# Kernel tuning notes

Measured on AMD Instinct MI355X. Metric: run time of the kernel, lower is better.

Reference implementation:

```python
import jax, jax.numpy as jnp
import numpy as np


def _adaptive_pool_mat(n_in, n_out):
    # torch AdaptiveAvgPool2d bin edges: start=floor(i*n_in/n_out), end=ceil((i+1)*n_in/n_out)
    M = np.zeros((n_out, n_in), np.float32)
    for i in range(n_out):
        s = (i * n_in) // n_out
        e = -(-((i + 1) * n_in) // n_out)
        M[i, s:e] = 1.0 / (e - s)
    return jnp.asarray(M)


def _bilinear_mat(n_out, n_in):
    # torch F.interpolate bilinear, align_corners=False, as a (n_out, n_in) matrix
    M = np.zeros((n_out, n_in), np.float32)
    scale = n_in / n_out
    for i in range(n_out):
        src = max((i + 0.5) * scale - 0.5, 0.0)
        i0 = min(int(np.floor(src)), n_in - 1)
        w = src - i0
        i1 = min(i0 + 1, n_in - 1)
        M[i, i0] += 1.0 - w
        M[i, i1] += w
    return jnp.asarray(M)


def _bn(x, g, b, m, v):
    # inference-mode BatchNorm2d over channel axis 1 of (B,C,H,W)
    inv = g / jnp.sqrt(v + 1e-5)
    return x * inv[None, :, None, None] + (b - m * inv)[None, :, None, None]


def _selective_scan(u, delta, A, Bs, Cs, D):
    # u, delta: (B,K,Di,L); A: (K,Di,N); Bs, Cs: (B,K,N,L); D: (K,Di)
    def step(h, inp):
        u_l, d_l, B_l, C_l = inp  # (B,K,Di), (B,K,Di), (B,K,N), (B,K,N)
        h = h * jnp.exp(d_l[..., None] * A) + (d_l * u_l)[..., None] * B_l[:, :, None, :]
        return h, jnp.einsum('bkdn,bkn->bkd', h, C_l)

    h0 = jnp.zeros(u.shape[:3] + (A.shape[-1],), u.dtype)
    xs = (u.transpose(3, 0, 1, 2), delta.transpose(3, 0, 1, 2),
          Bs.transpose(3, 0, 1, 2), Cs.transpose(3, 0, 1, 2))
    _, ys = jax.lax.scan(step, h0, xs)  # ys: (L,B,K,Di)
    return ys.transpose(1, 2, 3, 0) + D[None, :, :, None] * u


def _ss2d(x, in_proj_w, conv_w, conv_b, x_proj_w, dt_w, dt_b, A_logs, Ds, ln_g, ln_b, out_proj_w):
    # x: (B,H,W,d_model); VMamba SS2D with K=4 scan directions
    B, H, W, _ = x.shape
    K, N = 4, 16
    R = dt_w.shape[-1]
    Di = in_proj_w.shape[0] // 2
    xz = jnp.einsum('bhwc,ec->bhwe', x, in_proj_w)
    xi, z = jnp.split(xz, 2, axis=-1)
    xc = xi.transpose(0, 3, 1, 2)  # (B,Di,H,W)
    xc = jax.lax.conv_general_dilated(xc, conv_w, (1, 1), [(1, 1), (1, 1)],
                                      dimension_numbers=('NCHW', 'OIHW', 'NCHW'),
                                      feature_group_count=Di)
    xc = jax.nn.silu(xc + conv_b[None, :, None, None])
    L = H * W
    x_hw = xc.reshape(B, Di, L)
    x_wh = xc.transpose(0, 1, 3, 2).reshape(B, Di, L)
    xs2 = jnp.stack([x_hw, x_wh], axis=1)
    xs4 = jnp.concatenate([xs2, jnp.flip(xs2, axis=-1)], axis=1)  # (B,4,Di,L)
    x_dbl = jnp.einsum('bkdl,kcd->bkcl', xs4, x_proj_w)
    dts, Bm, Cm = jnp.split(x_dbl, [R, R + N], axis=2)
    delta = jax.nn.softplus(jnp.einsum('bkrl,kdr->bkdl', dts, dt_w) + dt_b[None, :, :, None])
    A = -jnp.exp(A_logs).reshape(K, Di, N)
    out_y = _selective_scan(xs4, delta, A, Bm, Cm, Ds.reshape(K, Di))  # (B,4,Di,L)
    inv_y = jnp.flip(out_y[:, 2:4], axis=-1)
    wh_y = out_y[:, 1].reshape(B, Di, W, H).transpose(0, 1, 3, 2).reshape(B, Di, L)
    invwh_y = inv_y[:, 1].reshape(B, Di, W, H).transpose(0, 1, 3, 2).reshape(B, Di, L)
    y = out_y[:, 0] + inv_y[:, 0] + wh_y + invwh_y  # (B,Di,L)
    y = y.transpose(0, 2, 1).reshape(B, H, W, Di)
    mu = jnp.mean(y, -1, keepdims=True)
    var = jnp.var(y, -1, keepdims=True)
    y = (y - mu) / jnp.sqrt(var + 1e-5) * ln_g + ln_b  # out_norm (LayerNorm)
    y = y * jax.nn.silu(z)
    return jnp.einsum('bhwd,cd->bhwc', y, out_proj_w)


def _forward(x, pool_w, pool_b, bn_g, bn_b, bn_m, bn_v, in_proj_w, conv_w, conv_b,
             x_proj_w, dt_w, dt_b, A_logs, Ds, ln_g, ln_b, out_proj_w,
             cbr_w, cbr_b, cbr_g, cbr_beta, cbr_m, cbr_v):
    B, C, H, W = x.shape
    pool_scales = [1, 5, 9, 13]  # generate_arithmetic_sequence(1, 16, 4)
    outs = [x]
    # pool layer 0: conv1x1 -> BN -> ReLU -> global avg pool -> upsample (constant)
    y0 = jnp.einsum('bchw,dc->bdhw', x, pool_w[0]) + pool_b[0][None, :, None, None]
    y0 = jax.nn.relu(_bn(y0, bn_g[0], bn_b[0], bn_m[0], bn_v[0]))
    y0 = jnp.mean(y0, axis=(2, 3), keepdims=True)
    outs.append(jnp.broadcast_to(y0, (B, y0.shape[1], H, W)))
    # pool layers 1..3: adaptive avg pool -> conv1x1 -> BN -> ReLU -> bilinear upsample
    for i, s in enumerate(pool_scales[1:], start=1):
        Mh, Mw = _adaptive_pool_mat(H, s), _adaptive_pool_mat(W, s)
        p = jnp.einsum('bchw,ph,qw->bcpq', x, Mh, Mw)
        p = jnp.einsum('bcpq,dc->bdpq', p, pool_w[i]) + pool_b[i][None, :, None, None]
        p = jax.nn.relu(_bn(p, bn_g[i], bn_b[i], bn_m[i], bn_v[i]))
        Uh, Uw = _bilinear_mat(H, s), _bilinear_mat(W, s)
        outs.append(jnp.einsum('bcpq,hp,wq->bchw', p, Uh, Uw))
    feat = jnp.concatenate(outs, axis=1)  # (B, dim*4 + in_chs = 1024, H, W)
    y = _ss2d(feat.transpose(0, 2, 3, 1), in_proj_w, conv_w, conv_b, x_proj_w,
              dt_w, dt_b, A_logs, Ds, ln_g, ln_b, out_proj_w)
    y = y.transpose(0, 3, 1, 2)
    # cbr: conv1x1 -> BN -> GELU
    y = jnp.einsum('bchw,dc->bdhw', y, cbr_w) + cbr_b[None, :, None, None]
    y = _bn(y, cbr_g, cbr_beta, cbr_m, cbr_v)
    return jax.nn.gelu(y, approximate=False)


def setup_inputs():
    key = jax.random.key(0)
    ks = jax.random.split(key, 20)
    B, C, H, W = 4, 512, 16, 16
    dim, P = 128, 4
    dm = dim * P + C            # 1024
    Di, K, N, R = 2 * dm, 4, 16, dm // 16  # 2048, 4, 16, 64
    f = jax.random.normal
    return {
        'x': f(ks[0], (B, C, H, W), jnp.float32),
        'pool_w': f(ks[1], (P, dim, C), jnp.float32) * 0.05,
        'pool_b': f(ks[2], (P, dim), jnp.float32) * 0.05,
        'bn_g': jnp.ones((P, dim), jnp.float32),
        'bn_b': jnp.zeros((P, dim), jnp.float32),
        'bn_m': f(ks[3], (P, dim), jnp.float32) * 0.1,
        'bn_v': jax.random.uniform(ks[4], (P, dim), jnp.float32, 0.5, 1.5),
        'in_proj_w': f(ks[5], (2 * Di, dm), jnp.float32) * 0.02,
        'conv_w': f(ks[6], (Di, 1, 3, 3), jnp.float32) * 0.1,
        'conv_b': f(ks[7], (Di,), jnp.float32) * 0.05,
        'x_proj_w': f(ks[8], (K, R + 2 * N, Di), jnp.float32) * 0.02,
        'dt_w': f(ks[9], (K, Di, R), jnp.float32) * 0.05,
        'dt_b': f(ks[10], (K, Di), jnp.float32) * 0.1,
        'A_logs': jax.random.uniform(ks[11], (K * Di, N), jnp.float32),
        'Ds': f(ks[12], (K * Di,), jnp.float32) * 0.1,
        'ln_g': jnp.ones((Di,), jnp.float32),
        'ln_b': jnp.zeros((Di,), jnp.float32),
        'out_proj_w': f(ks[13], (dm, Di), jnp.float32) * 0.02,
        'cbr_w': f(ks[14], (dim, dm), jnp.float32) * 0.05,
        'cbr_b': f(ks[15], (dim,), jnp.float32) * 0.05,
        'cbr_g': jnp.ones((dim,), jnp.float32),
        'cbr_beta': jnp.zeros((dim,), jnp.float32),
        'cbr_m': f(ks[16], (dim,), jnp.float32) * 0.1,
        'cbr_v': jax.random.uniform(ks[17], (dim,), jnp.float32, 0.5, 1.5),
    }


def reference(x, pool_w, pool_b, bn_g, bn_b, bn_m, bn_v, in_proj_w, conv_w, conv_b,
              x_proj_w, dt_w, dt_b, A_logs, Ds, ln_g, ln_b, out_proj_w,
              cbr_w, cbr_b, cbr_g, cbr_beta, cbr_m, cbr_v):
    return _forward(x, pool_w, pool_b, bn_g, bn_b, bn_m, bn_v, in_proj_w, conv_w, conv_b,
                    x_proj_w, dt_w, dt_b, A_logs, Ds, ln_g, ln_b, out_proj_w,
                    cbr_w, cbr_b, cbr_g, cbr_beta, cbr_m, cbr_v)
```

## Files before the change

kernel.cpp:

```cpp
#include <hip/hip_runtime.h>
#include <hip/hip_bf16.h>
#include <math.h>

#define Bsz 4
#define Cin 512
#define Hh 16
#define Ww 16
#define Lsp 256
#define DIM 128
#define DM 1024
#define DI 2048
#define KK 4
#define NST 16
#define RR 64
#define PW 384
#define NCH 4
#define CHUNK 64

#define OFF_FEAT    0u
#define SZ_FEAT     (Bsz*Lsp*DM)
#define OFF_POOLED  (OFF_FEAT + SZ_FEAT)
#define SZ_POOLED   (Bsz*Cin*275)
#define OFF_PCONV   (OFF_POOLED + SZ_POOLED)
#define SZ_PCONV    (Bsz*275*DIM)
#define OFF_Y0M     (OFF_PCONV + SZ_PCONV)
#define SZ_Y0M      (Bsz*DIM)
#define OFF_XZ      (OFF_Y0M + SZ_Y0M)
#define SZ_XZ       (Bsz*Lsp*2*DI)
#define OFF_XCT     (OFF_XZ + SZ_XZ)
#define SZ_XCT      (Bsz*Lsp*DI)
#define OFF_XDBL    (OFF_XCT + SZ_XCT)
#define SZ_XDBL     (Bsz*Lsp*PW)
#define OFF_DELTA   (OFF_XDBL + SZ_XDBL)
#define SZ_DELTA    (Bsz*KK*Lsp*DI)
#define OFF_OUTY    (OFF_DELTA + SZ_DELTA)
#define SZ_OUTY     (Bsz*KK*Lsp*DI)
#define OFF_YG      (OFF_OUTY + SZ_OUTY)
#define SZ_YG       (Bsz*Lsp*DI)
#define OFF_O1      (OFF_YG + SZ_YG)
#define SZ_O1       (Bsz*Lsp*DM)
#define OFF_O2      (OFF_O1 + SZ_O1)
#define SZ_O2       (Bsz*Lsp*DIM)
#define WS_FLOATS   (OFF_O2 + SZ_O2)

typedef __attribute__((ext_vector_type(8))) short short8;
typedef __attribute__((ext_vector_type(4))) float f32x4;

__device__ __forceinline__ short f2bf(float x) {
  __hip_bfloat16 h = __float2bfloat16(x);
  short s;
  __builtin_memcpy(&s, &h, 2);
  return s;
}
__device__ __forceinline__ float bf2f(short s) {
  unsigned u = ((unsigned)(unsigned short)s) << 16;
  float f;
  __builtin_memcpy(&f, &u, 4);
  return f;
}
__device__ __forceinline__ float unpack_lo(unsigned v) {
  unsigned u = v << 16; float f; __builtin_memcpy(&f, &u, 4); return f;
}
__device__ __forceinline__ float unpack_hi(unsigned v) {
  unsigned u = v & 0xffff0000u; float f; __builtin_memcpy(&f, &u, 4); return f;
}

__global__ __launch_bounds__(256) void f2bf5_kernel(
    const float* __restrict__ s0, short* __restrict__ d0,
    const float* __restrict__ s1, short* __restrict__ d1,
    const float* __restrict__ s2, short* __restrict__ d2,
    const float* __restrict__ s3, short* __restrict__ d3,
    const float* __restrict__ s4, short* __restrict__ d4) {
  int blk = blockIdx.x;
  const float* src; short* dst; int base;
  if (blk < 2048)      { src = s0; dst = d0; base = blk; }
  else if (blk < 2432) { src = s1; dst = d1; base = blk - 2048; }
  else if (blk < 3456) { src = s2; dst = d2; base = blk - 2432; }
  else if (blk < 3520) { src = s3; dst = d3; base = blk - 3456; }
  else                 { src = s4; dst = d4; base = blk - 3520; }
  int i = (base*256 + threadIdx.x)*8;
  float4 a = *(const float4*)(src + i);
  float4 b = *(const float4*)(src + i + 4);
  short8 o;
  o[0]=f2bf(a.x); o[1]=f2bf(a.y); o[2]=f2bf(a.z); o[3]=f2bf(a.w);
  o[4]=f2bf(b.x); o[5]=f2bf(b.y); o[6]=f2bf(b.z); o[7]=f2bf(b.w);
  *(short8*)(dst + i) = o;
}

__global__ __launch_bounds__(256) void pool0_kernel(
    const float* __restrict__ x, const float* __restrict__ pw, const float* __restrict__ pb,
    const float* __restrict__ g, const float* __restrict__ bb,
    const float* __restrict__ m, const float* __restrict__ v, float* __restrict__ y0m) {
  int bd = blockIdx.x;
  int b = bd >> 7, d = bd & 127;
  int l = threadIdx.x;
  const float* xb = x + (b*Cin)*Lsp + l;
  const float* w = pw + d*Cin;
  float a0 = 0.f, a1 = 0.f, a2 = 0.f, a3 = 0.f;
  #pragma unroll 4
  for (int c = 0; c < Cin; c += 4) {
    float4 wv = *(const float4*)(w + c);
    a0 += xb[(c+0)*Lsp] * wv.x;
    a1 += xb[(c+1)*Lsp] * wv.y;
    a2 += xb[(c+2)*Lsp] * wv.z;
    a3 += xb[(c+3)*Lsp] * wv.w;
  }
  float s = (a0 + a1) + (a2 + a3) + pb[d];
  float inv = g[d] * rsqrtf(v[d] + 1e-5f);
  s = s*inv + (bb[d] - m[d]*inv);
  s = fmaxf(s, 0.f);
  __shared__ float red[256];
  red[l] = s; __syncthreads();
  for (int off = 128; off > 0; off >>= 1) {
    if (l < off) red[l] += red[l+off];
    __syncthreads();
  }
  if (l == 0) y0m[bd] = red[0] * (1.f/256.f);
}

__device__ __forceinline__ void decode_pos(int pos, int& s, int& pp, int& qq, int& layer) {
  if (pos < 25)       { s = 5;  layer = 1; int t = pos;       pp = t/5;  qq = t%5;  }
  else if (pos < 106) { s = 9;  layer = 2; int t = pos - 25;  pp = t/9;  qq = t%9;  }
  else                { s = 13; layer = 3; int t = pos - 106; pp = t/13; qq = t%13; }
}

__global__ void pool_avg_kernel(const float* __restrict__ x, float* __restrict__ pooled) {
  int bc = blockIdx.x;
  int pos = threadIdx.x;
  if (pos >= 275) return;
  int s, pp, qq, layer;
  decode_pos(pos, s, pp, qq, layer);
  int hs = (pp*Hh)/s, he = ((pp+1)*Hh + s-1)/s;
  int ws = (qq*Ww)/s, we = ((qq+1)*Ww + s-1)/s;
  const float* xb = x + (size_t)bc*Lsp;
  float acc = 0.f;
  for (int hh = hs; hh < he; ++hh)
    for (int ww2 = ws; ww2 < we; ++ww2)
      acc += xb[hh*Ww + ww2];
  pooled[(size_t)bc*275 + pos] = acc / (float)((he-hs)*(we-ws));
}

__global__ void pconv_kernel(const float* __restrict__ pooled, const float* __restrict__ pw,
    const float* __restrict__ pb, const float* __restrict__ g, const float* __restrict__ bb,
    const float* __restrict__ m, const float* __restrict__ v, float* __restrict__ pconv) {
  int bp = blockIdx.x;
  int b = bp / 275, pos = bp % 275;
  int d = threadIdx.x;
  int s, pp, qq, layer;
  decode_pos(pos, s, pp, qq, layer);
  const float* pc = pooled + b*Cin*275 + pos;
  const float* w = pw + (layer*DIM + d)*Cin;
  float a0 = 0.f, a1 = 0.f, a2 = 0.f, a3 = 0.f;
  #pragma unroll 4
  for (int c = 0; c < Cin; c += 4) {
    float4 wv = *(const float4*)(w + c);
    a0 += pc[(c+0)*275] * wv.x;
    a1 += pc[(c+1)*275] * wv.y;
    a2 += pc[(c+2)*275] * wv.z;
    a3 += pc[(c+3)*275] * wv.w;
  }
  float acc = (a0 + a1) + (a2 + a3) + pb[layer*DIM + d];
  int ld = layer*DIM + d;
  float inv = g[ld] * rsqrtf(v[ld] + 1e-5f);
  acc = acc*inv + (bb[ld] - m[ld]*inv);
  pconv[bp*DIM + d] = fmaxf(acc, 0.f);
}

__global__ __launch_bounds__(256) void xT_kernel(const float* __restrict__ x,
    short* __restrict__ featB) {
  int b = blockIdx.z;
  int c0 = blockIdx.x*32, l0 = blockIdx.y*32;
  __shared__ float t[32][33];
  int tx = threadIdx.x & 31, ty = threadIdx.x >> 5;
  #pragma unroll
  for (int i = 0; i < 4; ++i) {
    int c = c0 + ty + i*8;
    t[ty + i*8][tx] = x[((size_t)b*Cin + c)*Lsp + l0 + tx];
  }
  __syncthreads();
  #pragma unroll
  for (int i = 0; i < 4; ++i) {
    int l = l0 + ty + i*8;
    featB[(size_t)(b*Lsp + l)*DM + c0 + tx] = f2bf(t[tx][ty + i*8]);
  }
}

__global__ __launch_bounds__(256) void feat_fill(const float* __restrict__ y0m,
    const float* __restrict__ pconv, short* __restrict__ featB) {
  int bl = blockIdx.x;
  int b = bl >> 8, l = bl & 255;
  int h = l >> 4, w = l & 15;
  for (int cc = threadIdx.x; cc < 512; cc += 256) {
    float val;
    if (cc < 128) {
      val = y0m[b*DIM + cc];
    } else {
      int i = (cc - 128) >> 7;
      int d = (cc - 128) & 127;
      int s = (i==0) ? 5 : (i==1) ? 9 : 13;
      int off = (i==0) ? 0 : (i==1) ? 25 : 106;
      float scale = (float)s / 16.f;
      float sh = fmaxf((h + 0.5f)*scale - 0.5f, 0.f);
      int h0 = min((int)sh, s-1); float wh = sh - (float)h0; int h1 = min(h0+1, s-1);
      float sw = fmaxf((w + 0.5f)*scale - 0.5f, 0.f);
      int w0 = min((int)sw, s-1); float ww2 = sw - (float)w0; int w1 = min(w0+1, s-1);
      const float* pc = pconv + b*275*DIM;
      float v00 = pc[(off + h0*s + w0)*DIM + d];
      float v01 = pc[(off + h0*s + w1)*DIM + d];
      float v10 = pc[(off + h1*s + w0)*DIM + d];
      float v11 = pc[(off + h1*s + w1)*DIM + d];
      val = (1.f-wh)*((1.f-ww2)*v00 + ww2*v01) + wh*((1.f-ww2)*v10 + ww2*v11);
    }
    featB[(size_t)bl*DM + 512 + cc] = f2bf(val);
  }
}

__device__ __forceinline__ int dir_map(int k, int l) {
  if (k == 0) return l;
  if (k == 1) return ((l & 15) << 4) | (l >> 4);
  if (k == 2) return 255 - l;
  int m = 255 - l; return ((m & 15) << 4) | (m >> 4);
}
__device__ __forceinline__ int inv_map(int k, int sp) {
  int t = ((sp & 15) << 4) | (sp >> 4);
  if (k == 0) return sp;
  if (k == 1) return t;
  if (k == 2) return 255 - sp;
  return 255 - t;
}

__device__ __forceinline__ void gload_lds16(const short* g, short* l) {
  __builtin_amdgcn_global_load_lds((const __attribute__((address_space(1))) void*)g,
                                   (__attribute__((address_space(3))) void*)l, 16, 0, 0);
}

template<int MODE>
__global__ __launch_bounds__(256) void gemm_bf(const short* __restrict__ Ag,
    const short* __restrict__ Bg, void* __restrict__ Cout, const float* __restrict__ bias,
    int M, int N, int K, int lda, int ldb,
    int azs, int bzs, unsigned czs, int ezs,
    const short* __restrict__ xcb, void* __restrict__ aux) {
  __shared__ short Als[128*64];
  __shared__ short Bls[128*64];
  int kdir = blockIdx.z;
  Ag += (size_t)kdir * azs;
  Bg += (size_t)kdir * bzs;
  size_t cz = (size_t)kdir * czs;
  if (bias) bias += (size_t)kdir * ezs;
  int tid = threadIdx.x;
  int w = tid >> 6, lane = tid & 63;
  int wm = w >> 1, wn = w & 1;
  int row0 = blockIdx.y * 128, col0 = blockIdx.x * 128;
  f32x4 acc[4][4];
  #pragma unroll
  for (int i = 0; i < 4; ++i)
    #pragma unroll
    for (int j = 0; j < 4; ++j)
      acc[i][j] = (f32x4){0.f, 0.f, 0.f, 0.f};

  for (int k0 = 0; k0 < K; k0 += 64) {
    #pragma unroll
    for (int i = 0; i < 4; ++i) {
      int slot = i*256 + w*64 + lane;
      int r = slot >> 3, pc = slot & 7;
      int c = pc ^ (r & 7);
      gload_lds16(Ag + (size_t)(row0 + r)*lda + k0 + c*8, &Als[(i*256 + w*64)*8]);
      gload_lds16(Bg + (size_t)(col0 + r)*ldb + k0 + c*8, &Bls[(i*256 + w*64)*8]);
    }
    __syncthreads();
    #pragma unroll
    for (int ks = 0; ks < 2; ++ks) {
      short8 af[4], bfr[4];
      int rsel = lane & 15, csel = ks*4 + (lane >> 4);
      #pragma unroll
      for (int mi = 0; mi < 4; ++mi) {
        int row = wm*64 + mi*16 + rsel;
        af[mi] = *(const short8*)&Als[row*64 + ((csel ^ (row & 7)) << 3)];
      }
      #pragma unroll
      for (int ni = 0; ni < 4; ++ni) {
        int row = wn*64 + ni*16 + rsel;
        bfr[ni] = *(const short8*)&Bls[row*64 + ((csel ^ (row & 7)) << 3)];
      }
      #pragma unroll
      for (int mi = 0; mi < 4; ++mi)
        #pragma unroll
        for (int ni = 0; ni < 4; ++ni)
          acc[mi][ni] = __builtin_amdgcn_mfma_f32_16x16x32_bf16(af[mi], bfr[ni], acc[mi][ni], 0, 0, 0);
    }
    __syncthreads();
  }
  #pragma unroll
  for (int mi = 0; mi < 4; ++mi) {
    int rbase = row0 + wm*64 + mi*16 + ((lane >> 4) << 2);
    #pragma unroll
    for (int ni = 0; ni < 4; ++ni) {
      int colg = col0 + wn*64 + ni*16 + (lane & 15);
      #pragma unroll
      for (int j = 0; j < 4; ++j) {
        if (MODE == 1) {
          ((short*)Cout)[(size_t)(rbase + j)*N + colg] = f2bf(acc[mi][ni][j]);
        } else if (MODE == 4) {
          int rowg = rbase + j;
          int b_ = rowg >> 8, sp_ = rowg & 255;
          int lsc = inv_map(kdir, sp_);
          float dl = acc[mi][ni][j] + bias[colg];
          dl = (dl > 20.f) ? dl : log1pf(__expf(dl));
          float ul = bf2f(xcb[(size_t)rowg*N + colg]);
          unsigned pv = ((unsigned)(unsigned short)f2bf(dl*ul) << 16)
                      |  (unsigned)(unsigned short)f2bf(dl);
          ((unsigned*)Cout)[cz + (size_t)(b_*Lsp + lsc)*N + colg] = pv;
        } else if (MODE == 5) {
          float vv = acc[mi][ni][j];
          ((float*)Cout)[(size_t)(rbase + j)*N + colg] = vv;
          ((short*)aux)[(size_t)(rbase + j)*N + colg] = f2bf(vv);
        } else {
          ((float*)Cout)[(size_t)(rbase + j)*N + colg] = acc[mi][ni][j];
        }
      }
    }
  }
}

__global__ __launch_bounds__(256) void dwconv_kernel(const short* __restrict__ xzB,
    const float* __restrict__ cw, const float* __restrict__ cb, short* __restrict__ xcB) {
  int bl = blockIdx.x;
  int b = bl >> 8, l = bl & 255;
  int h = l >> 4, w = l & 15;
  const short* xzb = xzB + (size_t)b*Lsp*(2*DI);
  #pragma unroll
  for (int it = 0; it < 4; ++it) {
    int d = (threadIdx.x + it*256)*2;
    float s0 = cb[d], s1 = cb[d+1];
    #pragma unroll
    for (int dh = -1; dh <= 1; ++dh) {
      int hh = h + dh; if (hh < 0 || hh > 15) continue;
      #pragma unroll
      for (int dw = -1; dw <= 1; ++dw) {
        int ww2 = w + dw; if (ww2 < 0 || ww2 > 15) continue;
        int t = (dh+1)*3 + (dw+1);
        short2 xv = *(const short2*)&xzb[(size_t)(hh*16 + ww2)*(2*DI) + d];
        s0 += bf2f(xv.x) * cw[d*9 + t];
        s1 += bf2f(xv.y) * cw[(d+1)*9 + t];
      }
    }
    float r0 = s0 / (1.f + __expf(-s0));
    float r1 = s1 / (1.f + __expf(-s1));
    short2 o; o.x = f2bf(r0); o.y = f2bf(r1);
    *(short2*)&xcB[((size_t)b*Lsp + l)*DI + d] = o;
  }
}

__global__ __launch_bounds__(256) void ps_build(const float* __restrict__ P,
    float* __restrict__ PS) {
  int slab = blockIdx.x;
  int k = slab >> 2, b = slab & 3;
  int l = threadIdx.x;
  int sp = dir_map(k, l);
  const float* src = P + (size_t)(b*Lsp + sp)*PW + k*96 + RR;
  float* dst = PS + ((size_t)slab*Lsp + l)*32;
  #pragma unroll
  for (int n = 0; n < 32; n += 4)
    *(float4*)(dst + n) = *(const float4*)(src + n);
}

__global__ __launch_bounds__(256) void scan_pass1(const unsigned* __restrict__ pk,
    const float* __restrict__ PS, const float* __restrict__ A_logs,
    float* __restrict__ Pa, float* __restrict__ Hend, short* __restrict__ oyB) {
  int bk = blockIdx.x;
  int b = bk >> 2, k = bk & 3;
  int slab = k*Bsz + b;
  int tid = threadIdx.x;
  int wv = tid >> 6, lane = tid & 63;
  int dloc = lane >> 2, ng = lane & 3;
  int d = blockIdx.y*64 + wv*16 + dloc;
  int c = blockIdx.z;
  int n0 = ng*4;
  float A[4], h[4] = {0.f,0.f,0.f,0.f};
  float sdl = 0.f;
  #pragma unroll
  for (int j = 0; j < 4; ++j)
    A[j] = -__expf(A_logs[((size_t)k*DI + d)*NST + n0 + j]);
  const unsigned* pkp = pk + (size_t)slab*Lsp*DI;
  const float* ps  = PS + (size_t)slab*Lsp*32;
  if (c == 0) {
    short* oy = oyB + (size_t)bk*Lsp*DI;
    #pragma unroll 2
    for (int l = 0; l < CHUNK; ++l) {
      unsigned v = pkp[(size_t)l*DI + d];
      float dl = unpack_lo(v);
      float du = unpack_hi(v);
      sdl += dl;
      float4 Bv = *(const float4*)(ps + l*32 + n0);
      float4 Cv = *(const float4*)(ps + l*32 + 16 + n0);
      float y;
      float e0 = __expf(dl*A[0]); h[0] = h[0]*e0 + du*Bv.x; y  = h[0]*Cv.x;
      float e1 = __expf(dl*A[1]); h[1] = h[1]*e1 + du*Bv.y; y += h[1]*Cv.y;
      float e2 = __expf(dl*A[2]); h[2] = h[2]*e2 + du*Bv.z; y += h[2]*Cv.z;
      float e3 = __expf(dl*A[3]); h[3] = h[3]*e3 + du*Bv.w; y += h[3]*Cv.w;
      y += __shfl_xor(y, 1);
      y += __shfl_xor(y, 2);
      if (ng == 0) oy[(size_t)l*DI + d] = f2bf(y);
    }
  } else {
    #pragma unroll 2
    for (int l = c*CHUNK; l < (c+1)*CHUNK; ++l) {
      unsigned v = pkp[(size_t)l*DI + d];
      float dl = unpack_lo(v);
      float du = unpack_hi(v);
      sdl += dl;
      float4 Bv = *(const float4*)(ps + l*32 + n0);
      float e0 = __expf(dl*A[0]); h[0] = h[0]*e0 + du*Bv.x;
      float e1 = __expf(dl*A[1]); h[1] = h[1]*e1 + du*Bv.y;
      float e2 = __expf(dl*A[2]); h[2] = h[2]*e2 + du*Bv.z;
      float e3 = __expf(dl*A[3]); h[3] = h[3]*e3 + du*Bv.w;
    }
  }
  size_t base = ((size_t)(c*16 + bk)*DI + d)*NST + n0;
  #pragma unroll
  for (int j = 0; j < 4; ++j) {
    Pa[base + j] = __expf(A[j]*sdl);
    Hend[base + j] = h[j];
  }
}

__global__ __launch_bounds__(256) void scan_combine(const float* __restrict__ Pa,
    const float* __restrict__ Hend, float* __restrict__ Hstart) {
  int idx = blockIdx.x*256 + threadIdx.x;
  const int stride = 16*DI*NST;
  float h = 0.f;
  #pragma unroll
  for (int c = 0; c < NCH; ++c) {
    Hstart[c*stride + idx] = h;
    h = Pa[c*stride + idx]*h + Hend[c*stride + idx];
  }
}

__global__ __launch_bounds__(256) void scan_pass2(const unsigned* __restrict__ pk,
    const float* __restrict__ PS, const float* __restrict__ A_logs,
    const float* __restrict__ Hstart, short* __restrict__ oyB) {
  int bk = blockIdx.x;
  int b = bk >> 2, k = bk & 3;
  int slab = k*Bsz + b;
  int tid = threadIdx.x;
  int wv = tid >> 6, lane = tid & 63;
  int dloc = lane >> 2, ng = lane & 3;
  int d = blockIdx.y*64 + wv*16 + dloc;
  int c = blockIdx.z + 1;
  int n0 = ng*4;
  float A[4], h[4];
  #pragma unroll
  for (int j = 0; j < 4; ++j)
    A[j] = -__expf(A_logs[((size_t)k*DI + d)*NST + n0 + j]);
  size_t hbase = ((size_t)(c*16 + bk)*DI + d)*NST + n0;
  #pragma unroll
  for (int j = 0; j < 4; ++j) h[j] = Hstart[hbase + j];
  const unsigned* pkp = pk + (size_t)slab*Lsp*DI;
  const float* ps  = PS + (size_t)slab*Lsp*32;
  short* oy = oyB + (size_t)bk*Lsp*DI;
  #pragma unroll 2
  for (int l = c*CHUNK; l < (c+1)*CHUNK; ++l) {
    unsigned v = pkp[(size_t)l*DI + d];
    float dl = unpack_lo(v);
    float du = unpack_hi(v);
    float4 Bv = *(const float4*)(ps + l*32 + n0);
    float4 Cv = *(const float4*)(ps + l*32 + 16 + n0);
    float y;
    float e0 = __expf(dl*A[0]); h[0] = h[0]*e0 + du*Bv.x; y  = h[0]*Cv.x;
    float e1 = __expf(dl*A[1]); h[1] = h[1]*e1 + du*Bv.y; y += h[1]*Cv.y;
    float e2 = __expf(dl*A[2]); h[2] = h[2]*e2 + du*Bv.z; y += h[2]*Cv.z;
    float e3 = __expf(dl*A[3]); h[3] = h[3]*e3 + du*Bv.w; y += h[3]*Cv.w;
    y += __shfl_xor(y, 1);
    y += __shfl_xor(y, 2);
    if (ng == 0) oy[(size_t)l*DI + d] = f2bf(y);
  }
}

__global__ __launch_bounds__(256) void combine_ln_kernel(const short* __restrict__ oyB,
    const short* __restrict__ xzB, const short* __restrict__ xcB,
    const float* __restrict__ Ds, const float* __restrict__ lng,
    const float* __restrict__ lnb, short* __restrict__ ygB) {
  int bl = blockIdx.x;
  int b = bl >> 8, l = bl & 255;
  int h = l >> 4, w = l & 15;
  int lT = (w << 4) | h;
  const short* oy = oyB + (size_t)b*KK*Lsp*DI;
  float vals[8];
  float sum = 0.f, sumsq = 0.f;
  #pragma unroll
  for (int i = 0; i < 8; ++i) {
    int d = threadIdx.x + i*256;
    float dsum = Ds[d] + Ds[DI + d] + Ds[2*DI + d] + Ds[3*DI + d];
    float yv = bf2f(oy[(size_t)(0*Lsp + l       )*DI + d])
             + bf2f(oy[(size_t)(2*Lsp + (255-l ))*DI + d])
             + bf2f(oy[(size_t)(1*Lsp + lT      )*DI + d])
             + bf2f(oy[(size_t)(3*Lsp + (255-lT))*DI + d])
             + bf2f(xcB[(size_t)bl*DI + d]) * dsum;
    vals[i] = yv; sum += yv; sumsq += yv*yv;
  }
  __shared__ float r1[256], r2[256];
  r1[threadIdx.x] = sum; r2[threadIdx.x] = sumsq; __syncthreads();
  for (int off = 128; off > 0; off >>= 1) {
    if (threadIdx.x < off) { r1[threadIdx.x] += r1[threadIdx.x+off]; r2[threadIdx.x] += r2[threadIdx.x+off]; }
    __syncthreads();
  }
  float mu = r1[0] * (1.f/2048.f);
  float var = r2[0] * (1.f/2048.f) - mu*mu;
  float rstd = rsqrtf(var + 1e-5f);
  const short* zrow = xzB + (size_t)bl*(2*DI) + DI;
  #pragma unroll
  for (int i = 0; i < 8; ++i) {
    int d = threadIdx.x + i*256;
    float z = bf2f(zrow[d]);
    float sz = z / (1.f + __expf(-z));
    ygB[(size_t)bl*DI + d] = f2bf(((vals[i]-mu)*rstd*lng[d] + lnb[d]) * sz);
  }
}

__global__ void cbr_epilogue(const float* __restrict__ o2, const float* __restrict__ cb,
    const float* __restrict__ g, const float* __restrict__ beta, const float* __restrict__ m_,
    const float* __restrict__ v_, float* __restrict__ out) {
  int idx = blockIdx.x*256 + threadIdx.x;
  int l = idx & 255;
  int rest = idx >> 8;
  int dd = rest & 127;
  int b = rest >> 7;
  float s = o2[((size_t)b*Lsp + l)*DIM + dd] + cb[dd];
  float inv = g[dd] * rsqrtf(v_[dd] + 1e-5f);
  s = s*inv + (beta[dd] - m_[dd]*inv);
  out[idx] = s * 0.5f * (1.f + erff(s * 0.70710678118f));
}

extern "C" void kernel_launch(void* const* d_in, const int* in_sizes, int n_in,
                              void* d_out, int out_size, void* d_ws, size_t ws_size,
                              hipStream_t stream) {
  const float* x        = (const float*)d_in[0];
  const float* pool_w   = (const float*)d_in[1];
  const float* pool_b   = (const float*)d_in[2];
  const float* bn_g     = (const float*)d_in[3];
  const float* bn_b     = (const float*)d_in[4];
  const float* bn_m     = (const float*)d_in[5];
  const float* bn_v     = (const float*)d_in[6];
  const float* in_proj_w= (const float*)d_in[7];
  const float* conv_w   = (const float*)d_in[8];
  const float* conv_b   = (const float*)d_in[9];
  const float* x_proj_w = (const float*)d_in[10];
  const float* dt_w     = (const float*)d_in[11];
  const float* dt_b     = (const float*)d_in[12];
  const float* A_logs   = (const float*)d_in[13];
  const float* Ds       = (const float*)d_in[14];
  const float* ln_g     = (const float*)d_in[15];
  const float* ln_b     = (const float*)d_in[16];
  const float* out_proj_w=(const float*)d_in[17];
  const float* cbr_w    = (const float*)d_in[18];
  const float* cbr_b    = (const float*)d_in[19];
  const float* cbr_g    = (const float*)d_in[20];
  const float* cbr_beta = (const float*)d_in[21];
  const float* cbr_m    = (const float*)d_in[22];
  const float* cbr_v    = (const float*)d_in[23];
  float* out = (float*)d_out;

  if (ws_size < (size_t)WS_FLOATS * sizeof(float)) return;
  float* ws = (float*)d_ws;
  float* pooled   = ws + OFF_POOLED;
  float* pconv    = ws + OFF_PCONV;
  float* y0m      = ws + OFF_Y0M;
  float* P        = ws + OFF_XDBL;
  unsigned* pk    = (unsigned*)(ws + OFF_DELTA);
  float* o2       = ws + OFF_O2;

  short* featB = (short*)(ws + OFF_POOLED);
  float* PS    = ws + OFF_POOLED;
  short* xzB   = (short*)(ws + OFF_XZ);
  short* wInB  = (short*)(ws + OFF_DELTA);
  short* wXB   = (short*)(ws + OFF_DELTA + 2097152);
  short* wOB   = (short*)(ws + OFF_FEAT);
  short* wCB   = (short*)(ws + OFF_PCONV);
  short* xcB   = (short*)(ws + OFF_O1);
  short* oyB   = (short*)(ws + OFF_OUTY);
  float* Pa    = ws + OFF_OUTY + 4194304;
  float* Hend  = ws + OFF_OUTY + 4194304 + 2097152;
  short* dtwB  = (short*)(ws + OFF_OUTY + 4194304);
  short* PB    = (short*)(ws + OFF_OUTY + 4194304 + 262144);
  float* Hstart= ws + OFF_YG;
  short* ygB   = (short*)(ws + OFF_DELTA);
  short* o1B   = (short*)(ws + OFF_O1);

  pool0_kernel<<<Bsz*DIM, 256, 0, stream>>>(x, pool_w, pool_b, bn_g, bn_b, bn_m, bn_v, y0m);
  pool_avg_kernel<<<Bsz*Cin, 288, 0, stream>>>(x, pooled);
  pconv_kernel<<<Bsz*275, 128, 0, stream>>>(pooled, pool_w, pool_b, bn_g, bn_b, bn_m, bn_v, pconv);
  xT_kernel<<<dim3(16, 8, Bsz), 256, 0, stream>>>(x, featB);
  feat_fill<<<Bsz*Lsp, 256, 0, stream>>>(y0m, pconv, featB);

  f2bf5_kernel<<<3776, 256, 0, stream>>>(in_proj_w, wInB, x_proj_w, wXB,
      out_proj_w, wOB, cbr_w, wCB, dt_w, dtwB);

  gemm_bf<1><<<dim3(32, 8, 1), 256, 0, stream>>>(featB, wInB, xzB, nullptr,
      1024, 4096, 1024, 1024, 1024, 0, 0, 0, 0, nullptr, nullptr);

  dwconv_kernel<<<Bsz*Lsp, 256, 0, stream>>>(xzB, conv_w, conv_b, xcB);

  gemm_bf<5><<<dim3(3, 8, 1), 256, 0, stream>>>(xcB, wXB, P, nullptr,
      1024, PW, 2048, 2048, 2048, 0, 0, 0, 0, nullptr, PB);
  ps_build<<<16, 256, 0, stream>>>(P, PS);

  gemm_bf<4><<<dim3(16, 8, KK), 256, 0, stream>>>(PB, dtwB, pk, dt_b,
      1024, DI, 64, PW, RR, 96, DI*RR, (unsigned)(Bsz*Lsp*DI), DI, xcB, nullptr);

  scan_pass1<<<dim3(Bsz*KK, DI/64, NCH), 256, 0, stream>>>(pk, PS, A_logs, Pa, Hend, oyB);
  scan_combine<<<(16*DI*NST)/256, 256, 0, stream>>>(Pa, Hend, Hstart);
  scan_pass2<<<dim3(Bsz*KK, DI/64, NCH-1), 256, 0, stream>>>(pk, PS, A_logs, Hstart, oyB);

  combine_ln_kernel<<<Bsz*Lsp, 256, 0, stream>>>(oyB, xzB, xcB, Ds, ln_g, ln_b, ygB);

  gemm_bf<1><<<dim3(8, 8, 1), 256, 0, stream>>>(ygB, wOB, o1B, nullptr,
      1024, 1024, 2048, 2048, 2048, 0, 0, 0, 0, nullptr, nullptr);

  gemm_bf<0><<<dim3(1, 8, 1), 256, 0, stream>>>(o1B, wCB, o2, nullptr,
      1024, DIM, 1024, 1024, 1024, 0, 0, 0, 0, nullptr, nullptr);
  cbr_epilogue<<<(Bsz*DIM*Lsp)/256, 256, 0, stream>>>(o2, cbr_b, cbr_g, cbr_beta, cbr_m, cbr_v, out);
}
```

Before: 347.3 us.

## Fuse chunked scan passes into one kernel with shared-memory chunk combine

Replaces the three-kernel chunked selective scan (pass1, global combine, pass2) with one kernel. Each block covers 16 channels, and each of its four waves handles one sequence chunk. Chunk end states and decay products go through shared memory and are combined after a block barrier, so the Pa/Hend/Hstart global round trips and two launches disappear. The last wave prefetches its chunk's inputs into cache while the others run pass 1. The softplus also switches from log1pf to the faster __logf(1+exp), which gives up some accuracy for small values.

```diff
diff --git a/kernel.cpp b/kernel.cpp
--- a/kernel.cpp
+++ b/kernel.cpp
@@ -305,7 +305,7 @@
           int b_ = rowg >> 8, sp_ = rowg & 255;
           int lsc = inv_map(kdir, sp_);
           float dl = acc[mi][ni][j] + bias[colg];
-          dl = (dl > 20.f) ? dl : log1pf(__expf(dl));
+          dl = (dl > 20.f) ? dl : __logf(1.f + __expf(dl));
           float ul = bf2f(xcb[(size_t)rowg*N + colg]);
           unsigned pv = ((unsigned)(unsigned short)f2bf(dl*ul) << 16)
                       |  (unsigned)(unsigned short)f2bf(dl);
@@ -364,33 +364,34 @@
     *(float4*)(dst + n) = *(const float4*)(src + n);
 }
 
-__global__ __launch_bounds__(256) void scan_pass1(const unsigned* __restrict__ pk,
+__global__ __launch_bounds__(256) void scan_fused(const unsigned* __restrict__ pk,
     const float* __restrict__ PS, const float* __restrict__ A_logs,
-    float* __restrict__ Pa, float* __restrict__ Hend, short* __restrict__ oyB) {
+    short* __restrict__ oyB) {
   int bk = blockIdx.x;
   int b = bk >> 2, k = bk & 3;
   int slab = k*Bsz + b;
   int tid = threadIdx.x;
   int wv = tid >> 6, lane = tid & 63;
   int dloc = lane >> 2, ng = lane & 3;
-  int d = blockIdx.y*64 + wv*16 + dloc;
-  int c = blockIdx.z;
+  int d = blockIdx.y*16 + dloc;
   int n0 = ng*4;
-  float A[4], h[4] = {0.f,0.f,0.f,0.f};
-  float sdl = 0.f;
+  __shared__ float sHend[3][16][16];
+  __shared__ float sPa[2][16][16];
+  float A[4];
   #pragma unroll
   for (int j = 0; j < 4; ++j)
     A[j] = -__expf(A_logs[((size_t)k*DI + d)*NST + n0 + j]);
   const unsigned* pkp = pk + (size_t)slab*Lsp*DI;
   const float* ps  = PS + (size_t)slab*Lsp*32;
-  if (c == 0) {
-    short* oy = oyB + (size_t)bk*Lsp*DI;
+  short* oy = oyB + (size_t)bk*Lsp*DI;
+  float h[4] = {0.f,0.f,0.f,0.f};
+
+  if (wv == 0) {
     #pragma unroll 2
     for (int l = 0; l < CHUNK; ++l) {
       unsigned v = pkp[(size_t)l*DI + d];
       float dl = unpack_lo(v);
       float du = unpack_hi(v);
-      sdl += dl;
       float4 Bv = *(const float4*)(ps + l*32 + n0);
       float4 Cv = *(const float4*)(ps + l*32 + 16 + n0);
       float y;
@@ -402,7 +403,11 @@
       y += __shfl_xor(y, 2);
       if (ng == 0) oy[(size_t)l*DI + d] = f2bf(y);
     }
-  } else {
+    #pragma unroll
+    for (int j = 0; j < 4; ++j) sHend[0][dloc][n0+j] = h[j];
+  } else if (wv <= 2) {
+    int c = wv;
+    float sdl = 0.f;
     #pragma unroll 2
     for (int l = c*CHUNK; l < (c+1)*CHUNK; ++l) {
       unsigned v = pkp[(size_t)l*DI + d];
@@ -415,64 +420,45 @@
       float e2 = __expf(dl*A[2]); h[2] = h[2]*e2 + du*Bv.z;
       float e3 = __expf(dl*A[3]); h[3] = h[3]*e3 + du*Bv.w;
     }
-  }
-  size_t base = ((size_t)(c*16 + bk)*DI + d)*NST + n0;
-  #pragma unroll
-  for (int j = 0; j < 4; ++j) {
-    Pa[base + j] = __expf(A[j]*sdl);
-    Hend[base + j] = h[j];
-  }
-}
-
-__global__ __launch_bounds__(256) void scan_combine(const float* __restrict__ Pa,
-    const float* __restrict__ Hend, float* __restrict__ Hstart) {
-  int idx = blockIdx.x*256 + threadIdx.x;
-  const int stride = 16*DI*NST;
-  float h = 0.f;
-  #pragma unroll
-  for (int c = 0; c < NCH; ++c) {
-    Hstart[c*stride + idx] = h;
-    h = Pa[c*stride + idx]*h + Hend[c*stride + idx];
-  }
-}
-
-__global__ __launch_bounds__(256) void scan_pass2(const unsigned* __restrict__ pk,
-    const float* __restrict__ PS, const float* __restrict__ A_logs,
-    const float* __restrict__ Hstart, short* __restrict__ oyB) {
-  int bk = blockIdx.x;
-  int b = bk >> 2, k = bk & 3;
-  int slab = k*Bsz + b;
-  int tid = threadIdx.x;
-  int wv = tid >> 6, lane = tid & 63;
-  int dloc = lane >> 2, ng = lane & 3;
-  int d = blockIdx.y*64 + wv*16 + dloc;
-  int c = blockIdx.z + 1;
-  int n0 = ng*4;
-  float A[4], h[4];
-  #pragma unroll
-  for (int j = 0; j < 4; ++j)
-    A[j] = -__expf(A_logs[((size_t)k*DI + d)*NST + n0 + j]);
-  size_t hbase = ((size_t)(c*16 + bk)*DI + d)*NST + n0;
-  #pragma unroll
-  for (int j = 0; j < 4; ++j) h[j] = Hstart[hbase + j];
-  const unsigned* pkp = pk + (size_t)slab*Lsp*DI;
-  const float* ps  = PS + (size_t)slab*Lsp*32;
-  short* oy = oyB + (size_t)bk*Lsp*DI;
-  #pragma unroll 2
-  for (int l = c*CHUNK; l < (c+1)*CHUNK; ++l) {
-    unsigned v = pkp[(size_t)l*DI + d];
-    float dl = unpack_lo(v);
-    float du = unpack_hi(v);
-    float4 Bv = *(const float4*)(ps + l*32 + n0);
-    float4 Cv = *(const float4*)(ps + l*32 + 16 + n0);
-    float y;
-    float e0 = __expf(dl*A[0]); h[0] = h[0]*e0 + du*Bv.x; y  = h[0]*Cv.x;
-    float e1 = __expf(dl*A[1]); h[1] = h[1]*e1 + du*Bv.y; y += h[1]*Cv.y;
-    float e2 = __expf(dl*A[2]); h[2] = h[2]*e2 + du*Bv.z; y += h[2]*Cv.z;
-    float e3 = __expf(dl*A[3]); h[3] = h[3]*e3 + du*Bv.w; y += h[3]*Cv.w;
-    y += __shfl_xor(y, 1);
-    y += __shfl_xor(y, 2);
-    if (ng == 0) oy[(size_t)l*DI + d] = f2bf(y);
+    #pragma unroll
+    for (int j = 0; j < 4; ++j) {
+      sHend[c][dloc][n0+j] = h[j];
+      sPa[c-1][dloc][n0+j] = __expf(A[j]*sdl);
+    }
+  } else {
+    unsigned ua = 0u; float fa = 0.f;
+    for (int l = 3*CHUNK; l < 4*CHUNK; l += 2) {
+      ua += pkp[(size_t)l*DI + d];
+      fa += ps[l*32 + (lane & 31)];
+    }
+    asm volatile("" :: "v"(ua), "v"(fa));
+  }
+  __syncthreads();
+  if (wv >= 1) {
+    int c = wv;
+    #pragma unroll
+    for (int j = 0; j < 4; ++j) {
+      float hh = sHend[0][dloc][n0+j];
+      if (c >= 2) hh = sPa[0][dloc][n0+j]*hh + sHend[1][dloc][n0+j];
+      if (c == 3) hh = sPa[1][dloc][n0+j]*hh + sHend[2][dloc][n0+j];
+      h[j] = hh;
+    }
+    #pragma unroll 2
+    for (int l = c*CHUNK; l < (c+1)*CHUNK; ++l) {
+      unsigned v = pkp[(size_t)l*DI + d];
+      float dl = unpack_lo(v);
+      float du = unpack_hi(v);
+      float4 Bv = *(const float4*)(ps + l*32 + n0);
+      float4 Cv = *(const float4*)(ps + l*32 + 16 + n0);
+      float y;
+      float e0 = __expf(dl*A[0]); h[0] = h[0]*e0 + du*Bv.x; y  = h[0]*Cv.x;
+      float e1 = __expf(dl*A[1]); h[1] = h[1]*e1 + du*Bv.y; y += h[1]*Cv.y;
+      float e2 = __expf(dl*A[2]); h[2] = h[2]*e2 + du*Bv.z; y += h[2]*Cv.z;
+      float e3 = __expf(dl*A[3]); h[3] = h[3]*e3 + du*Bv.w; y += h[3]*Cv.w;
+      y += __shfl_xor(y, 1);
+      y += __shfl_xor(y, 2);
+      if (ng == 0) oy[(size_t)l*DI + d] = f2bf(y);
+    }
   }
 }
 
@@ -578,11 +564,8 @@
   short* wCB   = (short*)(ws + OFF_PCONV);
   short* xcB   = (short*)(ws + OFF_O1);
   short* oyB   = (short*)(ws + OFF_OUTY);
-  float* Pa    = ws + OFF_OUTY + 4194304;
-  float* Hend  = ws + OFF_OUTY + 4194304 + 2097152;
   short* dtwB  = (short*)(ws + OFF_OUTY + 4194304);
   short* PB    = (short*)(ws + OFF_OUTY + 4194304 + 262144);
-  float* Hstart= ws + OFF_YG;
   short* ygB   = (short*)(ws + OFF_DELTA);
   short* o1B   = (short*)(ws + OFF_O1);
 
@@ -607,9 +590,7 @@
   gemm_bf<4><<<dim3(16, 8, KK), 256, 0, stream>>>(PB, dtwB, pk, dt_b,
       1024, DI, 64, PW, RR, 96, DI*RR, (unsigned)(Bsz*Lsp*DI), DI, xcB, nullptr);
 
-  scan_pass1<<<dim3(Bsz*KK, DI/64, NCH), 256, 0, stream>>>(pk, PS, A_logs, Pa, Hend, oyB);
-  scan_combine<<<(16*DI*NST)/256, 256, 0, stream>>>(Pa, Hend, Hstart);
-  scan_pass2<<<dim3(Bsz*KK, DI/64, NCH-1), 256, 0, stream>>>(pk, PS, A_logs, Hstart, oyB);
+  scan_fused<<<dim3(Bsz*KK, DI/16), 256, 0, stream>>>(pk, PS, A_logs, oyB);
 
   combine_ln_kernel<<<Bsz*Lsp, 256, 0, stream>>>(oyB, xzB, xcB, Ds, ln_g, ln_b, ygB);
 
```

Measured after the change: 317.3 us. -8.7%, faster.
